# Kernel optimization log

Hardware: AMD Instinct MI355X
Metric: run time of the kernel (lower is better)

## Reference

```python
import jax, jax.numpy as jnp
import numpy as np

N_QUBITS = 10
N_QLAYERS = 4
INV_SQRT2 = 1.0 / np.sqrt(2.0)


def setup_inputs() -> dict:
    key = jax.random.key(0)
    k1, k2 = jax.random.split(key)
    x = jax.random.normal(k1, (16, 256, 2 * N_QUBITS), dtype=jnp.float32)
    weights = jax.random.uniform(k2, (N_QLAYERS, N_QUBITS, 3), dtype=jnp.float32,
                                 minval=-np.pi, maxval=np.pi)
    return {"x": x, "weights": weights}


def _ry_mat(t):
    # t: scalar or (B,) -> (...,2,2) complex64 rotation about Y
    c = jnp.cos(t * 0.5)
    s = jnp.sin(t * 0.5)
    row0 = jnp.stack([c, -s], axis=-1)
    row1 = jnp.stack([s, c], axis=-1)
    return jnp.stack([row0, row1], axis=-2).astype(jnp.complex64)


def _rz_mat(p):
    # t: scalar or (B,) -> (...,2,2) complex64 diag(e^{-ip/2}, e^{+ip/2})
    e = jnp.exp(-0.5j * p.astype(jnp.complex64))
    z = jnp.zeros_like(e)
    row0 = jnp.stack([e, z], axis=-1)
    row1 = jnp.stack([z, jnp.conj(e)], axis=-1)
    return jnp.stack([row0, row1], axis=-2)


def _apply_1q(state, U, wire):
    # state: (B, 2,...,2); U: (2,2) shared or (B,2,2) per-sample
    ax = wire + 1
    s = jnp.moveaxis(state, ax, -1)
    if U.ndim == 3:
        s = jnp.einsum('bij,b...j->b...i', U, s)
    else:
        s = jnp.einsum('ij,...j->...i', U, s)
    return jnp.moveaxis(s, -1, ax)


def _apply_cnot(state, ctrl, tgt):
    a, b = ctrl + 1, tgt + 1
    s0 = jax.lax.index_in_dim(state, 0, axis=a, keepdims=True)
    s1 = jax.lax.index_in_dim(state, 1, axis=a, keepdims=True)
    s1 = jnp.flip(s1, axis=b)  # X on target within control=1 block
    return jnp.concatenate([s0, s1], axis=a)


def _circuit(x_flat, weights):
    n = N_QUBITS
    Bf = x_flat.shape[0]
    theta = jnp.pi * (x_flat[:, :n] + 1.0) * 0.5
    phi = jnp.pi * (x_flat[:, n:2 * n] + 1.0) * 0.5
    H = jnp.array([[1.0, 1.0], [1.0, -1.0]], dtype=jnp.complex64) * INV_SQRT2

    # |0...0> batched statevector: (Bf, 2, ..., 2)
    state = jnp.zeros((Bf, 2 ** n), dtype=jnp.complex64).at[:, 0].set(1.0)
    state = state.reshape((Bf,) + (2,) * n)

    # encoding layer
    for i in range(n):
        state = _apply_1q(state, H, i)
        state = _apply_1q(state, _ry_mat(theta[:, i]), i)
        state = _apply_1q(state, _rz_mat(phi[:, i]), i)

    # variational layers
    for layer in range(N_QLAYERS):
        for i in range(n):
            state = _apply_1q(state, _rz_mat(weights[layer, i, 0]), i)
            state = _apply_1q(state, _ry_mat(weights[layer, i, 1]), i)
            state = _apply_1q(state, _rz_mat(weights[layer, i, 2]), i)
        off = 1 if layer % 2 == 0 else n // 2
        for i in range(n):
            state = _apply_cnot(state, i, (i + off) % n)

    # <Z_i> = sum |amp|^2 * (+1 if qubit i = 0 else -1)
    probs = state.real ** 2 + state.imag ** 2
    zs = []
    for i in range(n):
        p = jnp.moveaxis(probs, i + 1, -1).reshape(Bf, -1, 2)
        zs.append(p[..., 0].sum(-1) - p[..., 1].sum(-1))
    return jnp.stack(zs, axis=-1)  # (Bf, n_qubits)


def reference(x, weights):
    B, L, _ = x.shape
    out = _circuit(x.reshape(-1, 2 * N_QUBITS), weights)
    return out.reshape(B, L, N_QUBITS)
```

## Files before the change

### kernel.cpp

```cpp
#include <hip/hip_runtime.h>
#include <math.h>

#define NQ 10
#define NLAYERS 4
#define NGATES (NLAYERS * NQ)

typedef float v2f __attribute__((ext_vector_type(2)));
typedef float v4f __attribute__((ext_vector_type(4)));

__device__ __forceinline__ v2f mk2(float a, float b) { v2f r; r.x = a; r.y = b; return r; }

__device__ __forceinline__ v2f cmul_m(v4f m, v2f s) {
    v2f r = m.xy * s;
    return __builtin_elementwise_fma(m.zw, s.yx, r);
}
__device__ __forceinline__ v2f cfma_m(v2f acc, v4f m, v2f s) {
    acc = __builtin_elementwise_fma(m.xy, s, acc);
    acc = __builtin_elementwise_fma(m.zw, s.yx, acc);
    return acc;
}
__device__ __forceinline__ v2f cmul(v2f a, v2f b) {
    v2f r = a.xx * b;
    return __builtin_elementwise_fma(mk2(-a.y, a.y), b.yx, r);
}
__device__ __forceinline__ v4f pack_u(float re, float im) {
    v4f m; m.x = re; m.y = re; m.z = -im; m.w = im; return m;
}

__host__ __device__ constexpr int pxor1(int v) {
    int y = v; y ^= y >> 1; y ^= y >> 2; y ^= y >> 4; y ^= y >> 8;
    return (y & 0x1FF) | (((y ^ (v >> 9)) & 1) << 9);
}
__host__ __device__ constexpr int pxor5(int v) {
    int lo = v & 31, hi = (v >> 5) & 31;
    return (lo << 5) | (lo ^ hi);
}

__device__ __forceinline__ void apply_gate(v2f* st, const v4f* __restrict__ M, int b) {
    v4f m0 = M[0], m1 = M[1], m2 = M[2], m3 = M[3];
    #pragma unroll
    for (int g = 0; g < 16; ++g) {
        int r0 = ((g >> b) << (b + 1)) | (g & ((1 << b) - 1));
        int r1 = r0 | (1 << b);
        v2f s0v = st[r0], s1v = st[r1];
        v2f n0 = cmul_m(m0, s0v); n0 = cfma_m(n0, m1, s1v);
        v2f n1 = cmul_m(m2, s0v); n1 = cfma_m(n1, m3, s1v);
        st[r0] = n0; st[r1] = n1;
    }
}

__device__ __forceinline__ void load_contig(v2f* st, const v2f* scratch, int lane) {
    const v4f* rp = (const v4f*)(scratch + 34 * lane);
    #pragma unroll
    for (int k = 0; k < 16; ++k) { v4f t = rp[k]; st[2 * k] = t.xy; st[2 * k + 1] = t.zw; }
}

__global__ void setup_mats(const float* __restrict__ w, v4f* __restrict__ mats) {
    int g = threadIdx.x;
    if (g >= NGATES) return;
    float w0 = w[g * 3 + 0], w1 = w[g * 3 + 1], w2 = w[g * 3 + 2];
    float hs = 0.5f * (w0 + w2), hd = 0.5f * (w0 - w2), hy = 0.5f * w1;
    float cy, sy, cs, ss, cd, sd;
    sincosf(hy, &sy, &cy);
    sincosf(hs, &ss, &cs);
    sincosf(hd, &sd, &cd);
    mats[g * 4 + 0] = pack_u( cy * cs, -cy * ss);
    mats[g * 4 + 1] = pack_u(-sy * cd, -sy * sd);
    mats[g * 4 + 2] = pack_u( sy * cd, -sy * sd);
    mats[g * 4 + 3] = pack_u( cy * cs,  cy * ss);
}

__global__ __launch_bounds__(64) void qsim_kernel(const float* __restrict__ x,
                                                  const v4f* __restrict__ mats,
                                                  float* __restrict__ out)
{
    __shared__ __align__(16) v2f scratch[2176];
    __shared__ __align__(16) v2f encf[2][NQ][2];

    const int lane = threadIdx.x;
    const int s = lane >> 5, sl = lane & 31;
    const int sample = 2 * blockIdx.x + s;

    if (sl < NQ) {
        const float* xs = x + (long)sample * (2 * NQ);
        float th = 0.7853981633974483f * (xs[sl] + 1.0f);
        float ph = 0.7853981633974483f * (xs[NQ + sl] + 1.0f);
        float cy, sy, cp, sp;
        sincosf(th, &sy, &cy);
        sincosf(ph, &sp, &cp);
        const float inv = 0.7071067811865476f;
        float a = (cy - sy) * inv, b = (cy + sy) * inv;
        v4f e; e.x = cp * a; e.y = -sp * a; e.z = cp * b; e.w = sp * b;
        *(v4f*)&encf[s][sl][0] = e;
    }
    __syncthreads();

    v2f st[32];
    {
        v2f P = encf[s][0][(sl >> 4) & 1];
        P = cmul(P, encf[s][1][(sl >> 3) & 1]);
        P = cmul(P, encf[s][2][(sl >> 2) & 1]);
        P = cmul(P, encf[s][3][(sl >> 1) & 1]);
        P = cmul(P, encf[s][4][sl & 1]);
        v4f e5 = *(const v4f*)&encf[s][5][0];
        v4f e6 = *(const v4f*)&encf[s][6][0];
        v4f e7 = *(const v4f*)&encf[s][7][0];
        v4f e8 = *(const v4f*)&encf[s][8][0];
        v4f e9 = *(const v4f*)&encf[s][9][0];
        v2f P5[2] = { cmul(P, e5.xy), cmul(P, e5.zw) };
        v2f t67[4], t89[4];
        t67[0] = cmul(e6.xy, e7.xy); t67[1] = cmul(e6.xy, e7.zw);
        t67[2] = cmul(e6.zw, e7.xy); t67[3] = cmul(e6.zw, e7.zw);
        t89[0] = cmul(e8.xy, e9.xy); t89[1] = cmul(e8.xy, e9.zw);
        t89[2] = cmul(e8.zw, e9.xy); t89[3] = cmul(e8.zw, e9.zw);
        v2f Q[8];
        #pragma unroll
        for (int a2 = 0; a2 < 2; ++a2)
            #pragma unroll
            for (int b2 = 0; b2 < 4; ++b2)
                Q[(a2 << 2) | b2] = cmul(P5[a2], t67[b2]);
        #pragma unroll
        for (int r = 0; r < 32; ++r)
            st[r] = cmul(Q[r >> 2], t89[r & 3]);
    }

    const int jb1 = pxor1(sl), jb5 = pxor5(sl);

    #pragma unroll
    for (int l = 0; l < NLAYERS; ++l) {
        #pragma unroll
        for (int q = 5; q <= 9; ++q)
            apply_gate(st, mats + (l * NQ + q) * 4, 9 - q);

        __syncthreads();
        {
            v2f* wp = scratch + 1088 * s + sl;
            #pragma unroll
            for (int r = 0; r < 32; ++r) wp[34 * r] = st[r];
        }
        __syncthreads();
        load_contig(st, scratch, lane);

        #pragma unroll
        for (int q = 0; q <= 4; ++q)
            apply_gate(st, mats + (l * NQ + q) * 4, 4 - q);

        __syncthreads();
        #pragma unroll
        for (int r = 0; r < 32; ++r) {
            const int jc = (l & 1) ? pxor5(r << 5) : pxor1(r << 5);
            const int jb = (l & 1) ? jb5 : jb1;
            const int j = jc ^ jb;
            scratch[1088 * s + j + 2 * (j >> 5)] = st[r];
        }
        __syncthreads();
        load_contig(st, scratch, lane);
    }

    {
        float p[32];
        #pragma unroll
        for (int r = 0; r < 32; ++r) {
            v2f a = st[r];
            v2f sq = a * a;
            p[r] = sq.x + sq.y;
        }
        float t0 = 0.f, t1 = 0.f, t2 = 0.f, t3 = 0.f, t4 = 0.f;
        float s0a[16], s1a[8], s2a[4], s3a[2];
        #pragma unroll
        for (int k = 0; k < 16; ++k) { s0a[k] = p[2*k] + p[2*k+1]; t0 += p[2*k] - p[2*k+1]; }
        #pragma unroll
        for (int k = 0; k < 8; ++k)  { s1a[k] = s0a[2*k] + s0a[2*k+1]; t1 += s0a[2*k] - s0a[2*k+1]; }
        #pragma unroll
        for (int k = 0; k < 4; ++k)  { s2a[k] = s1a[2*k] + s1a[2*k+1]; t2 += s1a[2*k] - s1a[2*k+1]; }
        #pragma unroll
        for (int k = 0; k < 2; ++k)  { s3a[k] = s2a[2*k] + s2a[2*k+1]; t3 += s2a[2*k] - s2a[2*k+1]; }
        float S = s3a[0] + s3a[1];   t4 = s3a[0] - s3a[1];

        float acc[NQ];
        #pragma unroll
        for (int q = 0; q < 5; ++q)
            acc[q] = ((sl >> (4 - q)) & 1) ? -S : S;
        acc[5] = t4; acc[6] = t3; acc[7] = t2; acc[8] = t1; acc[9] = t0;

        #pragma unroll
        for (int q = 0; q < NQ; ++q) {
            #pragma unroll
            for (int o = 16; o >= 1; o >>= 1)
                acc[q] += __shfl_xor(acc[q], o);
        }
        float v = acc[0];
        #pragma unroll
        for (int q = 1; q < NQ; ++q) v = (sl == q) ? acc[q] : v;
        if (sl < NQ)
            out[(long)sample * NQ + sl] = v;
    }
}

extern "C" void kernel_launch(void* const* d_in, const int* in_sizes, int n_in,
                              void* d_out, int out_size, void* d_ws, size_t ws_size,
                              hipStream_t stream) {
    const float* x = (const float*)d_in[0];
    const float* w = (const float*)d_in[1];
    float* out = (float*)d_out;
    v4f* mats = (v4f*)d_ws;
    const int n_samples = in_sizes[0] / (2 * NQ);
    setup_mats<<<1, 64, 0, stream>>>(w, mats);
    qsim_kernel<<<n_samples / 2, 64, 0, stream>>>(x, mats, out);
}
```

Baseline: 82.69 us.

## Fuse gate-matrix setup into main kernel and fold first variational layer into encoding

Removes the separate setup_mats launch: every block now computes the 40 fused rotation matrices into shared memory and reads them from LDS instead of global memory. The first variational layer is folded into the per-qubit product-state encoding, because before any CNOT the state is a product state, so layer 0's single-qubit gates can be applied to each qubit's 2-vector directly. This also changes the initial state layout, which adds an extra permuting shuffle and requires sign flips for the low qubits in the final reduction. The cost is redundant trig per block and extra shared-memory use.

```diff
diff --git a/kernel.cpp b/kernel.cpp
--- a/kernel.cpp
+++ b/kernel.cpp
@@ -55,34 +55,34 @@
     for (int k = 0; k < 16; ++k) { v4f t = rp[k]; st[2 * k] = t.xy; st[2 * k + 1] = t.zw; }
 }
 
-__global__ void setup_mats(const float* __restrict__ w, v4f* __restrict__ mats) {
-    int g = threadIdx.x;
-    if (g >= NGATES) return;
-    float w0 = w[g * 3 + 0], w1 = w[g * 3 + 1], w2 = w[g * 3 + 2];
-    float hs = 0.5f * (w0 + w2), hd = 0.5f * (w0 - w2), hy = 0.5f * w1;
-    float cy, sy, cs, ss, cd, sd;
-    sincosf(hy, &sy, &cy);
-    sincosf(hs, &ss, &cs);
-    sincosf(hd, &sd, &cd);
-    mats[g * 4 + 0] = pack_u( cy * cs, -cy * ss);
-    mats[g * 4 + 1] = pack_u(-sy * cd, -sy * sd);
-    mats[g * 4 + 2] = pack_u( sy * cd, -sy * sd);
-    mats[g * 4 + 3] = pack_u( cy * cs,  cy * ss);
-}
-
 __global__ __launch_bounds__(64) void qsim_kernel(const float* __restrict__ x,
-                                                  const v4f* __restrict__ mats,
+                                                  const float* __restrict__ w,
                                                   float* __restrict__ out)
 {
     __shared__ __align__(16) v2f scratch[2176];
+    __shared__ __align__(16) v4f matsL[NGATES * 4];
     __shared__ __align__(16) v2f encf[2][NQ][2];
 
     const int lane = threadIdx.x;
     const int s = lane >> 5, sl = lane & 31;
-    const int sample = 2 * blockIdx.x + s;
+    const long sample = 2L * blockIdx.x + s;
+
+    if (lane < NGATES) {
+        float w0 = w[lane * 3 + 0], w1 = w[lane * 3 + 1], w2 = w[lane * 3 + 2];
+        float hs = 0.5f * (w0 + w2), hd = 0.5f * (w0 - w2), hy = 0.5f * w1;
+        float cy, sy, cs, ss, cd, sd;
+        sincosf(hy, &sy, &cy);
+        sincosf(hs, &ss, &cs);
+        sincosf(hd, &sd, &cd);
+        matsL[lane * 4 + 0] = pack_u( cy * cs, -cy * ss);
+        matsL[lane * 4 + 1] = pack_u(-sy * cd, -sy * sd);
+        matsL[lane * 4 + 2] = pack_u( sy * cd, -sy * sd);
+        matsL[lane * 4 + 3] = pack_u( cy * cs,  cy * ss);
+    }
+    __syncthreads();
 
     if (sl < NQ) {
-        const float* xs = x + (long)sample * (2 * NQ);
+        const float* xs = x + sample * (2 * NQ);
         float th = 0.7853981633974483f * (xs[sl] + 1.0f);
         float ph = 0.7853981633974483f * (xs[NQ + sl] + 1.0f);
         float cy, sy, cp, sp;
@@ -90,47 +90,53 @@
         sincosf(ph, &sp, &cp);
         const float inv = 0.7071067811865476f;
         float a = (cy - sy) * inv, b = (cy + sy) * inv;
-        v4f e; e.x = cp * a; e.y = -sp * a; e.z = cp * b; e.w = sp * b;
-        *(v4f*)&encf[s][sl][0] = e;
+        v2f f0 = mk2(cp * a, -sp * a);
+        v2f f1 = mk2(cp * b,  sp * b);
+        v4f M0 = matsL[sl * 4 + 0], M1 = matsL[sl * 4 + 1];
+        v4f M2 = matsL[sl * 4 + 2], M3 = matsL[sl * 4 + 3];
+        encf[s][sl][0] = cfma_m(cmul_m(M0, f0), M1, f1);
+        encf[s][sl][1] = cfma_m(cmul_m(M2, f0), M3, f1);
     }
     __syncthreads();
 
     v2f st[32];
     {
-        v2f P = encf[s][0][(sl >> 4) & 1];
-        P = cmul(P, encf[s][1][(sl >> 3) & 1]);
-        P = cmul(P, encf[s][2][(sl >> 2) & 1]);
-        P = cmul(P, encf[s][3][(sl >> 1) & 1]);
-        P = cmul(P, encf[s][4][sl & 1]);
-        v4f e5 = *(const v4f*)&encf[s][5][0];
-        v4f e6 = *(const v4f*)&encf[s][6][0];
-        v4f e7 = *(const v4f*)&encf[s][7][0];
-        v4f e8 = *(const v4f*)&encf[s][8][0];
-        v4f e9 = *(const v4f*)&encf[s][9][0];
-        v2f P5[2] = { cmul(P, e5.xy), cmul(P, e5.zw) };
-        v2f t67[4], t89[4];
-        t67[0] = cmul(e6.xy, e7.xy); t67[1] = cmul(e6.xy, e7.zw);
-        t67[2] = cmul(e6.zw, e7.xy); t67[3] = cmul(e6.zw, e7.zw);
-        t89[0] = cmul(e8.xy, e9.xy); t89[1] = cmul(e8.xy, e9.zw);
-        t89[2] = cmul(e8.zw, e9.xy); t89[3] = cmul(e8.zw, e9.zw);
-        v2f Q[8];
-        #pragma unroll
-        for (int a2 = 0; a2 < 2; ++a2)
-            #pragma unroll
-            for (int b2 = 0; b2 < 4; ++b2)
-                Q[(a2 << 2) | b2] = cmul(P5[a2], t67[b2]);
+        v2f P = encf[s][5][(sl >> 4) & 1];
+        P = cmul(P, encf[s][6][(sl >> 3) & 1]);
+        P = cmul(P, encf[s][7][(sl >> 2) & 1]);
+        P = cmul(P, encf[s][8][(sl >> 1) & 1]);
+        P = cmul(P, encf[s][9][sl & 1]);
+        v2f q01[4], q23[4], q234[8], Pq[4];
+        #pragma unroll
+        for (int a2 = 0; a2 < 4; ++a2) {
+            q01[a2] = cmul(encf[s][0][(a2 >> 1) & 1], encf[s][1][a2 & 1]);
+            q23[a2] = cmul(encf[s][2][(a2 >> 1) & 1], encf[s][3][a2 & 1]);
+        }
+        #pragma unroll
+        for (int b2 = 0; b2 < 8; ++b2)
+            q234[b2] = cmul(q23[b2 >> 1], encf[s][4][b2 & 1]);
+        #pragma unroll
+        for (int a2 = 0; a2 < 4; ++a2) Pq[a2] = cmul(P, q01[a2]);
         #pragma unroll
         for (int r = 0; r < 32; ++r)
-            st[r] = cmul(Q[r >> 2], t89[r & 3]);
+            st[r] = cmul(Pq[r >> 3], q234[r & 7]);
     }
 
     const int jb1 = pxor1(sl), jb5 = pxor5(sl);
 
     #pragma unroll
-    for (int l = 0; l < NLAYERS; ++l) {
+    for (int r = 0; r < 32; ++r) {
+        const int j = pxor1(r << 5) ^ jb1;
+        scratch[1088 * s + 34 * (j >> 5) + (j & 31)] = st[r];
+    }
+    __syncthreads();
+    load_contig(st, scratch, lane);
+
+    #pragma unroll
+    for (int l = 1; l < NLAYERS; ++l) {
         #pragma unroll
         for (int q = 5; q <= 9; ++q)
-            apply_gate(st, mats + (l * NQ + q) * 4, 9 - q);
+            apply_gate(st, matsL + (l * NQ + q) * 4, 9 - q);
 
         __syncthreads();
         {
@@ -143,18 +149,19 @@
 
         #pragma unroll
         for (int q = 0; q <= 4; ++q)
-            apply_gate(st, mats + (l * NQ + q) * 4, 4 - q);
-
-        __syncthreads();
-        #pragma unroll
-        for (int r = 0; r < 32; ++r) {
-            const int jc = (l & 1) ? pxor5(r << 5) : pxor1(r << 5);
-            const int jb = (l & 1) ? jb5 : jb1;
-            const int j = jc ^ jb;
-            scratch[1088 * s + j + 2 * (j >> 5)] = st[r];
-        }
-        __syncthreads();
-        load_contig(st, scratch, lane);
+            apply_gate(st, matsL + (l * NQ + q) * 4, 4 - q);
+
+        if (l < NLAYERS - 1) {
+            __syncthreads();
+            #pragma unroll
+            for (int r = 0; r < 32; ++r) {
+                const int jc = (l & 1) ? pxor5(r << 5) : pxor1(r << 5);
+                const int j = jc ^ ((l & 1) ? jb5 : jb1);
+                scratch[1088 * s + 34 * (j >> 5) + (j & 31)] = st[r];
+            }
+            __syncthreads();
+            load_contig(st, scratch, lane);
+        }
     }
 
     {
@@ -181,7 +188,11 @@
         #pragma unroll
         for (int q = 0; q < 5; ++q)
             acc[q] = ((sl >> (4 - q)) & 1) ? -S : S;
-        acc[5] = t4; acc[6] = t3; acc[7] = t2; acc[8] = t1; acc[9] = t0;
+        acc[5] = ((sl >> 4) & 1) ? -t4 : t4;
+        acc[6] = ((sl >> 3) & 1) ? -t3 : t3;
+        acc[7] = ((sl >> 2) & 1) ? -t2 : t2;
+        acc[8] = ((sl >> 1) & 1) ? -t1 : t1;
+        acc[9] = (sl & 1)        ? -t0 : t0;
 
         #pragma unroll
         for (int q = 0; q < NQ; ++q) {
@@ -193,7 +204,7 @@
         #pragma unroll
         for (int q = 1; q < NQ; ++q) v = (sl == q) ? acc[q] : v;
         if (sl < NQ)
-            out[(long)sample * NQ + sl] = v;
+            out[sample * NQ + sl] = v;
     }
 }
 
@@ -203,8 +214,6 @@
     const float* x = (const float*)d_in[0];
     const float* w = (const float*)d_in[1];
     float* out = (float*)d_out;
-    v4f* mats = (v4f*)d_ws;
     const int n_samples = in_sizes[0] / (2 * NQ);
-    setup_mats<<<1, 64, 0, stream>>>(w, mats);
-    qsim_kernel<<<n_samples / 2, 64, 0, stream>>>(x, mats, out);
-}
+    qsim_kernel<<<n_samples / 2, 64, 0, stream>>>(x, w, out);
+}
```

Result: faster. 78.55 us (-5.0%).
